# Kernel tuning notes

Measured on AMD Instinct MI355X. Metric: run time of the kernel, lower is better.

The kernel has to match this reference:

```python
import jax, jax.numpy as jnp
import numpy as np

EPS = 1e-5
INF = 1e9
H, D = 16, 24  # no_heads, c_hidden

def layer_norm(x, w, b):
    mu = jnp.mean(x, axis=-1, keepdims=True)
    var = jnp.mean(jnp.square(x - mu), axis=-1, keepdims=True)
    return (x - mu) * jax.lax.rsqrt(var + EPS) * w + b

def setup_inputs() -> dict:
    key = jax.random.key(0)
    ks = jax.random.split(key, 12)
    B, N, Cq, Cz = 1, 1024, 384, 128
    s = 0.02
    return {
        "a": jax.random.normal(ks[0], (B, N, Cq), jnp.float32),
        "z": jax.random.normal(ks[1], (B, N, N, Cz), jnp.float32),
        "mask": jnp.ones((B, N), jnp.float32),
        "ln_a_w": jnp.ones((Cq,), jnp.float32),
        "ln_a_b": jnp.zeros((Cq,), jnp.float32),
        "ln_z_w": jnp.ones((Cz,), jnp.float32),
        "ln_z_b": jnp.zeros((Cz,), jnp.float32),
        "w_z": jax.random.normal(ks[2], (Cz, H), jnp.float32) * s,
        "wq": jax.random.normal(ks[3], (Cq, H * D), jnp.float32) * s,
        "wk": jax.random.normal(ks[4], (Cq, H * D), jnp.float32) * s,
        "wv": jax.random.normal(ks[5], (Cq, H * D), jnp.float32) * s,
        "wg": jax.random.normal(ks[6], (Cq, H * D), jnp.float32) * s,
        "bg": jnp.ones((H * D,), jnp.float32),
        "wo": jax.random.normal(ks[7], (H * D, Cq), jnp.float32) * s,
        "bo": jnp.zeros((Cq,), jnp.float32),
    }

def reference(a, z, mask, ln_a_w, ln_a_b, ln_z_w, ln_z_b, w_z, wq, wk, wv, wg, bg, wo, bo):
    B, N, Cq = a.shape
    a_ln = layer_norm(a, ln_a_w, ln_a_b)                      # [B,N,Cq]
    # pair bias: LN -> Linear(no bias) -> permute to [B,H,N,N]
    zb = layer_norm(z, ln_z_w, ln_z_b) @ w_z                  # [B,N,N,H]
    pair_bias = jnp.transpose(zb, (0, 3, 1, 2))               # [B,H,N,N]
    mask_bias = (INF * (mask - 1.0))[:, None, None, :]        # [B,1,1,N]
    q = (a_ln @ wq).reshape(B, N, H, D) * (D ** -0.5)
    k = (a_ln @ wk).reshape(B, N, H, D)
    v = (a_ln @ wv).reshape(B, N, H, D)
    logits = jnp.einsum("bqhd,bkhd->bhqk", q, k) + mask_bias + pair_bias
    attn = jax.nn.softmax(logits, axis=-1)
    o = jnp.einsum("bhqk,bkhd->bqhd", attn, v)                # [B,N,H,D]
    g = jax.nn.sigmoid(a_ln @ wg + bg).reshape(B, N, H, D)
    o = (g * o).reshape(B, N, H * D)
    return o @ wo + bo
```

## Files before the change

### kernel.cpp

```cpp
#include <hip/hip_runtime.h>
#include <hip/hip_bf16.h>

typedef float f32x4 __attribute__((ext_vector_type(4)));
typedef short s16x8 __attribute__((ext_vector_type(8)));

__device__ __forceinline__ unsigned short f2bf(float x){
  unsigned u = __float_as_uint(x);
  u += 0x7fffu + ((u >> 16) & 1u);
  return (unsigned short)(u >> 16);
}
__device__ __forceinline__ float bf2f(unsigned short h){
  return __uint_as_float(((unsigned)h) << 16);
}
__device__ __forceinline__ unsigned pk_bf(float a, float b){
  __hip_bfloat162 t = __float22bfloat162_rn(make_float2(a, b));
  return *reinterpret_cast<unsigned*>(&t);
}

__global__ __launch_bounds__(256) void prep_kernel(const float* __restrict__ a, const float* __restrict__ ln_a_w,
                             const float* __restrict__ ln_a_b, const float* __restrict__ lnzw,
                             const float* __restrict__ lnzb, const float* __restrict__ w_z,
                             const float* __restrict__ wq, const float* __restrict__ wk,
                             const float* __restrict__ wv, const float* __restrict__ wg,
                             const float* __restrict__ wo,
                             unsigned short* __restrict__ a_lnB, unsigned short* __restrict__ wBall,
                             unsigned short* __restrict__ wwB, float* __restrict__ TU,
                             unsigned short* __restrict__ qTp, unsigned short* __restrict__ kTp,
                             unsigned short* __restrict__ vTt){
  int bid = blockIdx.x, tid = threadIdx.x;
  if (bid < 180){
    __shared__ float t[64][65];
    int mat = bid/36, tt = bid - mat*36;
    int c0 = (tt % 6)*64, k0 = (tt / 6)*64;
    const float* src = mat == 0 ? wq : mat == 1 ? wk : mat == 2 ? wv : mat == 3 ? wg : wo;
    int r = tid >> 4, c4 = (tid & 15)*4;
    #pragma unroll
    for (int rr = 0; rr < 4; ++rr){
      float4 v = *(const float4*)(src + (size_t)(k0 + r + rr*16)*384 + c0 + c4);
      t[r + rr*16][c4+0] = v.x; t[r + rr*16][c4+1] = v.y;
      t[r + rr*16][c4+2] = v.z; t[r + rr*16][c4+3] = v.w;
    }
    __syncthreads();
    float scale = (mat == 0) ? 0.20412414523193154f : 1.f;
    int cc = tid >> 2, kp = (tid & 3)*16;
    unsigned ow[8];
    #pragma unroll
    for (int j = 0; j < 8; ++j)
      ow[j] = pk_bf(t[kp + 2*j][cc]*scale, t[kp + 2*j + 1][cc]*scale);
    unsigned short* dst = wBall + ((size_t)(mat*384 + c0 + cc)*384 + k0 + kp);
    *(uint4*)dst       = make_uint4(ow[0], ow[1], ow[2], ow[3]);
    *(uint4*)(dst + 8) = make_uint4(ow[4], ow[5], ow[6], ow[7]);
  } else if (bid < 436){
    int r = (bid - 180)*4 + (tid >> 6), l = tid & 63;
    const float* ap = a + (size_t)r*384;
    float x[6]; float s = 0.f, sq = 0.f;
    #pragma unroll
    for (int i = 0; i < 6; ++i){ x[i] = ap[i*64 + l]; s += x[i]; sq += x[i]*x[i]; }
    #pragma unroll
    for (int off = 32; off; off >>= 1){ s += __shfl_xor(s, off); sq += __shfl_xor(sq, off); }
    float mu = s*(1.f/384.f);
    float var = sq*(1.f/384.f) - mu*mu;
    float rs = rsqrtf(var + 1e-5f);
    #pragma unroll
    for (int i = 0; i < 6; ++i){ int c = i*64 + l; a_lnB[(size_t)r*384 + c] = f2bf((x[i]-mu)*rs*ln_a_w[c] + ln_a_b[c]); }
  } else if (bid == 436){
    if (tid < 128){
      float lw = lnzw[tid];
      #pragma unroll
      for (int h = 0; h < 16; ++h) wwB[tid*16 + h] = f2bf(lw * w_z[tid*16 + h]);
    }
    if (tid < 16){
      float T = 0.f, U = 0.f;
      for (int c = 0; c < 128; ++c){ T += lnzw[c]*w_z[c*16 + tid]; U += lnzb[c]*w_z[c*16 + tid]; }
      TU[tid] = T; TU[16 + tid] = U;
    }
  } else {
    int t = (bid - 437)*256 + tid;
    uint4 zv = make_uint4(0,0,0,0);
    if (t < 16384)      *(uint4*)(qTp + (size_t)t*32 + 24) = zv;
    else if (t < 32768) *(uint4*)(kTp + (size_t)(t - 16384)*32 + 24) = zv;
    else {
      int t2 = t - 32768;
      int h = t2 >> 10, w = t2 & 1023;
      *(uint4*)(vTt + ((size_t)h*32 + 24)*1024 + (size_t)w*8) = zv;
    }
  }
}

__global__ __launch_bounds__(256) void midfuse_kernel(const unsigned short* __restrict__ AB,
                                                      const unsigned short* __restrict__ wBt,
                                                      const float* __restrict__ bg,
                                                      unsigned short* __restrict__ qTp, unsigned short* __restrict__ kTp,
                                                      unsigned short* __restrict__ vTt, float* __restrict__ g,
                                                      const float* __restrict__ z, const unsigned short* __restrict__ wwB,
                                                      const float* __restrict__ TU, const float* __restrict__ mask,
                                                      unsigned short* __restrict__ pbM){
  __shared__ char smem[16384];
  int bid = blockIdx.x, tid = threadIdx.x;
  int wave = tid >> 6, lane = tid & 63, l15 = lane & 15, sub = lane >> 4;
  if (bid < 384){
    s16x8* Al8 = (s16x8*)smem;
    s16x8* Bl8 = (s16x8*)(smem + 8192);
    int bx = bid % 24, by = bid / 24;
    int n0 = bx*64, m0 = by*64;
    f32x4 acc[4];
    #pragma unroll
    for (int c = 0; c < 4; ++c) acc[c] = (f32x4){0.f,0.f,0.f,0.f};
    const s16x8* Ag = (const s16x8*)AB;
    const s16x8* Bg = (const s16x8*)wBt;
    for (int ks = 0; ks < 6; ++ks){
      int k0u = ks*8;
      #pragma unroll
      for (int j = 0; j < 2; ++j){
        int idx = tid*2 + j;
        int row = idx >> 3, u = idx & 7;
        Al8[row*8 + (u ^ (row & 7))] = Ag[(size_t)(m0 + row)*48 + k0u + u];
        Bl8[row*8 + (u ^ (row & 7))] = Bg[(size_t)(n0 + row)*48 + k0u + u];
      }
      __syncthreads();
      #pragma unroll
      for (int kk = 0; kk < 2; ++kk){
        int arow = wave*16 + l15;
        s16x8 af = Al8[arow*8 + ((kk*4 + sub) ^ (arow & 7))];
        #pragma unroll
        for (int c = 0; c < 4; ++c){
          int brow = c*16 + l15;
          s16x8 bf = Bl8[brow*8 + ((kk*4 + sub) ^ (brow & 7))];
          acc[c] = __builtin_amdgcn_mfma_f32_16x16x32_bf16(af, bf, acc[c], 0, 0, 0);
        }
      }
      __syncthreads();
    }
    int which = bx / 6;
    int cb = n0 - which*384;
    if (which == 3){
      #pragma unroll
      for (int c = 0; c < 4; ++c){
        int col = cb + c*16 + l15;
        #pragma unroll
        for (int r = 0; r < 4; ++r){
          int row = m0 + wave*16 + sub*4 + r;
          float t = acc[c][r] + bg[col];
          g[(size_t)row*384 + col] = 1.f/(1.f + __expf(-t));
        }
      }
    } else if (which == 2){
      #pragma unroll
      for (int c = 0; c < 4; ++c){
        int col = cb + c*16 + l15;
        int h = col/24, d = col - h*24;
        unsigned p0 = pk_bf(acc[c][0], acc[c][1]);
        unsigned p1 = pk_bf(acc[c][2], acc[c][3]);
        size_t base = ((size_t)h*32 + d)*1024 + (size_t)(m0 + wave*16 + sub*4);
        *(uint2*)(vTt + base) = make_uint2(p0, p1);
      }
    } else {
      unsigned short* dst = which == 0 ? qTp : kTp;
      #pragma unroll
      for (int c = 0; c < 4; ++c){
        int col = cb + c*16 + l15;
        int h = col/24, d = col - h*24;
        #pragma unroll
        for (int r = 0; r < 4; ++r){
          int row = m0 + wave*16 + sub*4 + r;
          dst[((size_t)(h << 10) + row)*32 + d] = f2bf(acc[c][r]);
        }
      }
    }
  } else {
    float* sums = (float*)smem;
    float* sqs  = sums + 64;
    float (*accT)[17] = (float(*)[17])(sqs + 64);
    int tb = bid - 384;
    int h = l15, subz = sub;
    s16x8 bfr[4];
    #pragma unroll
    for (int kc = 0; kc < 4; ++kc)
      #pragma unroll
      for (int j = 0; j < 8; ++j) bfr[kc][j] = (short)wwB[(kc*32 + subz*8 + j)*16 + h];
    s16x8 ones1;
    #pragma unroll
    for (int j = 0; j < 8; ++j) ones1[j] = (h == 0) ? (short)0x3F80 : (short)0;
    int eh = tid >> 4, epl0 = (tid & 15)*4;
    float Te = TU[eh], Ue = TU[16 + eh];
    int row = wave*16 + h;
    for (int it = 0; it < 4; ++it){
      int tile = tb + it*4096;
      size_t pairBase = (size_t)tile*64;
      const float* zrow = z + (pairBase + row)*128;
      f32x4 acc  = {0.f, 0.f, 0.f, 0.f};
      f32x4 accS = {0.f, 0.f, 0.f, 0.f};
      f32x4 accG = {0.f, 0.f, 0.f, 0.f};
      #pragma unroll
      for (int kc = 0; kc < 4; ++kc){
        f32x4 v0 = *(const f32x4*)(zrow + kc*32 + subz*8);
        f32x4 v1 = *(const f32x4*)(zrow + kc*32 + subz*8 + 4);
        union { unsigned u[4]; s16x8 s; } cv;
        cv.u[0] = pk_bf(v0.x, v0.y); cv.u[1] = pk_bf(v0.z, v0.w);
        cv.u[2] = pk_bf(v1.x, v1.y); cv.u[3] = pk_bf(v1.z, v1.w);
        s16x8 af = cv.s;
        acc  = __builtin_amdgcn_mfma_f32_16x16x32_bf16(af, bfr[kc], acc, 0, 0, 0);
        accS = __builtin_amdgcn_mfma_f32_16x16x32_bf16(af, ones1, accS, 0, 0, 0);
        accG = __builtin_amdgcn_mfma_f32_16x16x32_bf16(af, af, accG, 0, 0, 0);
      }
      #pragma unroll
      for (int r = 0; r < 4; ++r) accT[wave*16 + subz*4 + r][h] = acc[r];
      if (h == 0){
        #pragma unroll
        for (int r = 0; r < 4; ++r) sums[wave*16 + subz*4 + r] = accS[r];
      }
      if (subz == (h >> 2)){
        int r = h & 3;
        float vq = r == 0 ? accG[0] : r == 1 ? accG[1] : r == 2 ? accG[2] : accG[3];
        sqs[wave*16 + h] = vq;
      }
      __syncthreads();
      float mus[4], rss[4];
      #pragma unroll
      for (int rr = 0; rr < 4; ++rr){
        float mu = sums[epl0+rr]*(1.f/128.f);
        float var = sqs[epl0+rr]*(1.f/128.f) - mu*mu;
        mus[rr] = mu; rss[rr] = rsqrtf(var + 1e-5f);
      }
      size_t p0 = pairBase + epl0;
      int q = (int)(p0 >> 10), k0 = (int)(p0 & 1023);
      float4 mk = *(const float4*)(mask + k0);
      float bv[4];
      bv[0] = rss[0]*(accT[epl0+0][eh] - mus[0]*Te) + Ue + 1e9f*(mk.x - 1.f);
      bv[1] = rss[1]*(accT[epl0+1][eh] - mus[1]*Te) + Ue + 1e9f*(mk.y - 1.f);
      bv[2] = rss[2]*(accT[epl0+2][eh] - mus[2]*Te) + Ue + 1e9f*(mk.z - 1.f);
      bv[3] = rss[3]*(accT[epl0+3][eh] - mus[3]*Te) + Ue + 1e9f*(mk.w - 1.f);
      int qb = q >> 6, q64 = q & 63;
      int qg = q64 >> 4, subq = (q64 >> 2) & 3, rr2 = q64 & 3;
      int kkt = k0 >> 6, c = (k0 >> 4) & 3, l15k = k0 & 15;
      size_t cbase = ((((size_t)(eh*16 + qb)*16 + kkt)*4 + qg)*4 + c)*256 + (size_t)rr2;
      #pragma unroll
      for (int i = 0; i < 4; ++i)
        pbM[cbase + (size_t)(subq*16 + l15k + i)*4] = f2bf(bv[i]);
      __syncthreads();
    }
  }
}

__global__ __launch_bounds__(512) void attn_kernel(const unsigned short* __restrict__ qTp, const unsigned short* __restrict__ kTp,
                                                   const unsigned short* __restrict__ vTt, const unsigned short* __restrict__ pbM,
                                                   const float* __restrict__ g, unsigned short* __restrict__ ogB){
  __shared__ float lds[8192];
  int tid = threadIdx.x;
  int wave = tid >> 6, lane = tid & 63, l15 = lane & 15, sub = lane >> 4;
  int qb32 = blockIdx.x, h = blockIdx.y;
  int qg_l = wave & 1, kkq = wave >> 1;
  int qrow = qb32*32 + qg_l*16 + l15;
  s16x8 qf = *(const s16x8*)(qTp + ((size_t)(h << 10) + qrow)*32 + sub*8);
  f32x4 o0 = {0.f,0.f,0.f,0.f}, o1 = {0.f,0.f,0.f,0.f};
  float m[4] = {-1e30f,-1e30f,-1e30f,-1e30f}, l[4] = {0.f,0.f,0.f,0.f};
  char* Pb = (char*)(lds + wave*1024);
  const unsigned short* kBase = kTp + ((size_t)(h << 10))*32;
  const unsigned short* vBase = vTt + (size_t)h*32*1024;
  int qb64 = qb32 >> 1, qg4 = (qb32 & 1)*2 + qg_l;
  const unsigned short* pbW = pbM + (size_t)(h*16 + qb64)*16*4096 + (size_t)qg4*1024 + (size_t)lane*4;
  for (int t = 0; t < 4; ++t){
    int kkt = kkq*4 + t;
    int kk0 = kkt*64;
    const unsigned short* pbt = pbW + (size_t)kkt*4096;
    uint2 pv0 = *(const uint2*)(pbt + 0);
    uint2 pv1 = *(const uint2*)(pbt + 256);
    uint2 pv2 = *(const uint2*)(pbt + 512);
    uint2 pv3 = *(const uint2*)(pbt + 768);
    f32x4 s[4];
    #pragma unroll
    for (int c = 0; c < 4; ++c){
      s16x8 kf = *(const s16x8*)(kBase + (size_t)(kk0 + c*16 + l15)*32 + sub*8);
      s[c] = __builtin_amdgcn_mfma_f32_16x16x32_bf16(qf, kf, (f32x4){0.f,0.f,0.f,0.f}, 0, 0, 0);
    }
    {
      uint2 pv[4] = {pv0, pv1, pv2, pv3};
      #pragma unroll
      for (int c = 0; c < 4; ++c){
        s[c][0] += bf2f((unsigned short)(pv[c].x & 0xffff));
        s[c][1] += bf2f((unsigned short)(pv[c].x >> 16));
        s[c][2] += bf2f((unsigned short)(pv[c].y & 0xffff));
        s[c][3] += bf2f((unsigned short)(pv[c].y >> 16));
      }
    }
    #pragma unroll
    for (int r = 0; r < 4; ++r){
      float pm = fmaxf(fmaxf(s[0][r], s[1][r]), fmaxf(s[2][r], s[3][r]));
      pm = fmaxf(pm, __shfl_xor(pm, 1));
      pm = fmaxf(pm, __shfl_xor(pm, 2));
      pm = fmaxf(pm, __shfl_xor(pm, 4));
      pm = fmaxf(pm, __shfl_xor(pm, 8));
      float mn = fmaxf(m[r], pm);
      float corr = __expf(m[r] - mn);
      m[r] = mn;
      float ps = 0.f;
      #pragma unroll
      for (int c = 0; c < 4; ++c){ s[c][r] = __expf(s[c][r] - mn); ps += s[c][r]; }
      ps += __shfl_xor(ps, 1); ps += __shfl_xor(ps, 2);
      ps += __shfl_xor(ps, 4); ps += __shfl_xor(ps, 8);
      l[r] = l[r]*corr + ps;
      o0[r] *= corr; o1[r] *= corr;
    }
    #pragma unroll
    for (int c = 0; c < 4; ++c){
      #pragma unroll
      for (int r = 0; r < 4; ++r){
        int qq = sub*4 + r;
        int byte = ((qq*128 + (c*16 + l15)*2)) ^ ((qq & 7) << 4);
        *(short*)(Pb + byte) = (short)f2bf(s[c][r]);
      }
    }
    #pragma unroll
    for (int kh = 0; kh < 2; ++kh){
      int byteA = (l15*128 + kh*64 + sub*16) ^ ((l15 & 7) << 4);
      s16x8 pa = *(const s16x8*)(Pb + byteA);
      s16x8 vb0 = *(const s16x8*)(vBase + (size_t)l15*1024 + kk0 + kh*32 + sub*8);
      s16x8 vb1 = *(const s16x8*)(vBase + (size_t)(16 + l15)*1024 + kk0 + kh*32 + sub*8);
      o0 = __builtin_amdgcn_mfma_f32_16x16x32_bf16(pa, vb0, o0, 0, 0, 0);
      o1 = __builtin_amdgcn_mfma_f32_16x16x32_bf16(pa, vb1, o1, 0, 0, 0);
    }
  }
  {
    float* cw = lds + wave*1024 + lane*16;
    cw[0] = o0[0]; cw[1] = o0[1]; cw[2] = o0[2]; cw[3] = o0[3];
    cw[4] = o1[0]; cw[5] = o1[1]; cw[6] = o1[2]; cw[7] = o1[3];
    cw[8] = m[0]; cw[9] = m[1]; cw[10] = m[2]; cw[11] = m[3];
    cw[12] = l[0]; cw[13] = l[1]; cw[14] = l[2]; cw[15] = l[3];
  }
  __syncthreads();
  if (kkq == 0){
    #pragma unroll
    for (int k2 = 1; k2 < 4; ++k2){
      const float* c2 = lds + (size_t)(k2*2 + qg_l)*1024 + lane*16;
      #pragma unroll
      for (int r = 0; r < 4; ++r){
        float m2 = c2[8 + r], l2 = c2[12 + r];
        float nm = fmaxf(m[r], m2);
        float f1 = __expf(m[r] - nm), f2 = __expf(m2 - nm);
        l[r] = l[r]*f1 + l2*f2;
        o0[r] = o0[r]*f1 + c2[r]*f2;
        o1[r] = o1[r]*f1 + c2[4 + r]*f2;
        m[r] = nm;
      }
    }
    #pragma unroll
    for (int r = 0; r < 4; ++r){
      float inv = 1.f/l[r];
      int q = qb32*32 + qg_l*16 + sub*4 + r;
      size_t base = (size_t)q*384 + h*24;
      ogB[base + l15] = f2bf(g[base + l15]*o0[r]*inv);
      if (l15 < 8) ogB[base + 16 + l15] = f2bf(g[base + 16 + l15]*o1[r]*inv);
    }
  }
}

__global__ __launch_bounds__(256) void gemm_out(const unsigned short* __restrict__ AB,
                                                const unsigned short* __restrict__ wBo,
                                                const float* __restrict__ bo, float* __restrict__ dst){
  __shared__ short Al[64*8*8];
  __shared__ short Bl[64*8*8];
  int tid = threadIdx.x;
  int wave = tid >> 6, lane = tid & 63, l15 = lane & 15, sub = lane >> 4;
  int n0 = blockIdx.x*64, m0 = blockIdx.y*64;
  f32x4 acc[4];
  #pragma unroll
  for (int c = 0; c < 4; ++c) acc[c] = (f32x4){0.f,0.f,0.f,0.f};
  const s16x8* Ag = (const s16x8*)AB;
  const s16x8* Bg = (const s16x8*)wBo;
  s16x8* Al8 = (s16x8*)Al; s16x8* Bl8 = (s16x8*)Bl;
  for (int ks = 0; ks < 6; ++ks){
    int k0u = ks*8;
    #pragma unroll
    for (int j = 0; j < 2; ++j){
      int idx = tid*2 + j;
      int row = idx >> 3, u = idx & 7;
      Al8[row*8 + (u ^ (row & 7))] = Ag[(size_t)(m0 + row)*48 + k0u + u];
      Bl8[row*8 + (u ^ (row & 7))] = Bg[(size_t)(n0 + row)*48 + k0u + u];
    }
    __syncthreads();
    #pragma unroll
    for (int kk = 0; kk < 2; ++kk){
      int arow = wave*16 + l15;
      s16x8 af = Al8[arow*8 + ((kk*4 + sub) ^ (arow & 7))];
      #pragma unroll
      for (int c = 0; c < 4; ++c){
        int brow = c*16 + l15;
        s16x8 bf = Bl8[brow*8 + ((kk*4 + sub) ^ (brow & 7))];
        acc[c] = __builtin_amdgcn_mfma_f32_16x16x32_bf16(af, bf, acc[c], 0, 0, 0);
      }
    }
    __syncthreads();
  }
  #pragma unroll
  for (int c = 0; c < 4; ++c){
    int col = n0 + c*16 + l15;
    float b = bo[col];
    #pragma unroll
    for (int r = 0; r < 4; ++r){
      int row = m0 + wave*16 + sub*4 + r;
      dst[(size_t)row*384 + col] = acc[c][r] + b;
    }
  }
}

extern "C" void kernel_launch(void* const* d_in, const int* in_sizes, int n_in,
                              void* d_out, int out_size, void* d_ws, size_t ws_size,
                              hipStream_t stream){
  const float* a      = (const float*)d_in[0];
  const float* z      = (const float*)d_in[1];
  const float* mask   = (const float*)d_in[2];
  const float* ln_a_w = (const float*)d_in[3];
  const float* ln_a_b = (const float*)d_in[4];
  const float* ln_z_w = (const float*)d_in[5];
  const float* ln_z_b = (const float*)d_in[6];
  const float* w_z    = (const float*)d_in[7];
  const float* wq     = (const float*)d_in[8];
  const float* wk     = (const float*)d_in[9];
  const float* wv     = (const float*)d_in[10];
  const float* wg     = (const float*)d_in[11];
  const float* bg     = (const float*)d_in[12];
  const float* wo     = (const float*)d_in[13];
  const float* bo     = (const float*)d_in[14];

  char* ws = (char*)d_ws;
  unsigned short* a_lnB = (unsigned short*)(ws + ((size_t)0u));
  unsigned short* wBall = (unsigned short*)(ws + ((size_t)1u << 20));
  unsigned short* qTp   = (unsigned short*)(ws + ((size_t)4u << 20));
  unsigned short* kTp   = (unsigned short*)(ws + ((size_t)6u << 20));
  unsigned short* vTt   = (unsigned short*)(ws + ((size_t)8u << 20));
  float* g    = (float*)(ws + ((size_t)10u << 20));
  unsigned short* ogB = (unsigned short*)(ws + ((size_t)12u << 20));
  unsigned short* wwB = (unsigned short*)(ws + ((size_t)14u << 20));
  float* TU   = (float*)(ws + ((size_t)14u << 20) + 8192);
  unsigned short* pbM = (unsigned short*)(ws + ((size_t)24u << 20));

  hipLaunchKernelGGL(prep_kernel, dim3(629), dim3(256), 0, stream, a, ln_a_w, ln_a_b,
                     ln_z_w, ln_z_b, w_z, wq, wk, wv, wg, wo, a_lnB, wBall, wwB, TU, qTp, kTp, vTt);
  hipLaunchKernelGGL(midfuse_kernel, dim3(4480), dim3(256), 0, stream, a_lnB, wBall, bg,
                     qTp, kTp, vTt, g, z, wwB, TU, mask, pbM);
  hipLaunchKernelGGL(attn_kernel, dim3(32,16), dim3(512), 0, stream, qTp, kTp, vTt, pbM, g, ogB);
  hipLaunchKernelGGL(gemm_out, dim3(6,16), dim3(256), 0, stream, ogB, wBall + (size_t)4*384*384, bo, (float*)d_out);
}
```

Baseline: 173.6 us.

## Split fused projection/pair-bias kernel and retile z bias for packed stores

Splits the combined midfuse kernel into a separate QKVG projection GEMM and a pair-bias kernel. The new z-bias kernel tiles 4 query rows by 16 keys, so each thread writes four bias values for its head as one packed 8-byte store instead of four scattered 2-byte stores. The attention kernel now loads the K fragments for the next key tile one iteration ahead and fully unrolls the loop. The cost is one extra kernel launch, the loss of overlap between the small GEMM and the large z pass, and more registers held in the attention kernel.

```diff
diff --git a/kernel.cpp b/kernel.cpp
--- a/kernel.cpp
+++ b/kernel.cpp
@@ -87,158 +87,150 @@
   }
 }
 
-__global__ __launch_bounds__(256) void midfuse_kernel(const unsigned short* __restrict__ AB,
-                                                      const unsigned short* __restrict__ wBt,
-                                                      const float* __restrict__ bg,
-                                                      unsigned short* __restrict__ qTp, unsigned short* __restrict__ kTp,
-                                                      unsigned short* __restrict__ vTt, float* __restrict__ g,
-                                                      const float* __restrict__ z, const unsigned short* __restrict__ wwB,
-                                                      const float* __restrict__ TU, const float* __restrict__ mask,
-                                                      unsigned short* __restrict__ pbM){
-  __shared__ char smem[16384];
-  int bid = blockIdx.x, tid = threadIdx.x;
+__global__ __launch_bounds__(256) void qkvg_kernel(const unsigned short* __restrict__ AB,
+                                                   const unsigned short* __restrict__ wBt,
+                                                   const float* __restrict__ bg,
+                                                   unsigned short* __restrict__ qTp, unsigned short* __restrict__ kTp,
+                                                   unsigned short* __restrict__ vTt, float* __restrict__ g){
+  __shared__ short Al[64*8*8];
+  __shared__ short Bl[64*8*8];
+  int tid = threadIdx.x;
   int wave = tid >> 6, lane = tid & 63, l15 = lane & 15, sub = lane >> 4;
-  if (bid < 384){
-    s16x8* Al8 = (s16x8*)smem;
-    s16x8* Bl8 = (s16x8*)(smem + 8192);
-    int bx = bid % 24, by = bid / 24;
-    int n0 = bx*64, m0 = by*64;
-    f32x4 acc[4];
-    #pragma unroll
-    for (int c = 0; c < 4; ++c) acc[c] = (f32x4){0.f,0.f,0.f,0.f};
-    const s16x8* Ag = (const s16x8*)AB;
-    const s16x8* Bg = (const s16x8*)wBt;
-    for (int ks = 0; ks < 6; ++ks){
-      int k0u = ks*8;
-      #pragma unroll
-      for (int j = 0; j < 2; ++j){
-        int idx = tid*2 + j;
-        int row = idx >> 3, u = idx & 7;
-        Al8[row*8 + (u ^ (row & 7))] = Ag[(size_t)(m0 + row)*48 + k0u + u];
-        Bl8[row*8 + (u ^ (row & 7))] = Bg[(size_t)(n0 + row)*48 + k0u + u];
-      }
-      __syncthreads();
-      #pragma unroll
-      for (int kk = 0; kk < 2; ++kk){
-        int arow = wave*16 + l15;
-        s16x8 af = Al8[arow*8 + ((kk*4 + sub) ^ (arow & 7))];
-        #pragma unroll
-        for (int c = 0; c < 4; ++c){
-          int brow = c*16 + l15;
-          s16x8 bf = Bl8[brow*8 + ((kk*4 + sub) ^ (brow & 7))];
-          acc[c] = __builtin_amdgcn_mfma_f32_16x16x32_bf16(af, bf, acc[c], 0, 0, 0);
-        }
-      }
-      __syncthreads();
-    }
-    int which = bx / 6;
-    int cb = n0 - which*384;
-    if (which == 3){
+  int n0 = blockIdx.x*64, m0 = blockIdx.y*64;
+  f32x4 acc[4];
+  #pragma unroll
+  for (int c = 0; c < 4; ++c) acc[c] = (f32x4){0.f,0.f,0.f,0.f};
+  const s16x8* Ag = (const s16x8*)AB;
+  const s16x8* Bg = (const s16x8*)wBt;
+  s16x8* Al8 = (s16x8*)Al; s16x8* Bl8 = (s16x8*)Bl;
+  for (int ks = 0; ks < 6; ++ks){
+    int k0u = ks*8;
+    #pragma unroll
+    for (int j = 0; j < 2; ++j){
+      int idx = tid*2 + j;
+      int row = idx >> 3, u = idx & 7;
+      Al8[row*8 + (u ^ (row & 7))] = Ag[(size_t)(m0 + row)*48 + k0u + u];
+      Bl8[row*8 + (u ^ (row & 7))] = Bg[(size_t)(n0 + row)*48 + k0u + u];
+    }
+    __syncthreads();
+    #pragma unroll
+    for (int kk = 0; kk < 2; ++kk){
+      int arow = wave*16 + l15;
+      s16x8 af = Al8[arow*8 + ((kk*4 + sub) ^ (arow & 7))];
       #pragma unroll
       for (int c = 0; c < 4; ++c){
-        int col = cb + c*16 + l15;
-        #pragma unroll
-        for (int r = 0; r < 4; ++r){
-          int row = m0 + wave*16 + sub*4 + r;
-          float t = acc[c][r] + bg[col];
-          g[(size_t)row*384 + col] = 1.f/(1.f + __expf(-t));
-        }
-      }
-    } else if (which == 2){
-      #pragma unroll
-      for (int c = 0; c < 4; ++c){
-        int col = cb + c*16 + l15;
-        int h = col/24, d = col - h*24;
-        unsigned p0 = pk_bf(acc[c][0], acc[c][1]);
-        unsigned p1 = pk_bf(acc[c][2], acc[c][3]);
-        size_t base = ((size_t)h*32 + d)*1024 + (size_t)(m0 + wave*16 + sub*4);
-        *(uint2*)(vTt + base) = make_uint2(p0, p1);
-      }
-    } else {
-      unsigned short* dst = which == 0 ? qTp : kTp;
-      #pragma unroll
-      for (int c = 0; c < 4; ++c){
-        int col = cb + c*16 + l15;
-        int h = col/24, d = col - h*24;
-        #pragma unroll
-        for (int r = 0; r < 4; ++r){
-          int row = m0 + wave*16 + sub*4 + r;
-          dst[((size_t)(h << 10) + row)*32 + d] = f2bf(acc[c][r]);
-        }
-      }
+        int brow = c*16 + l15;
+        s16x8 bf = Bl8[brow*8 + ((kk*4 + sub) ^ (brow & 7))];
+        acc[c] = __builtin_amdgcn_mfma_f32_16x16x32_bf16(af, bf, acc[c], 0, 0, 0);
+      }
+    }
+    __syncthreads();
+  }
+  int which = blockIdx.x / 6;
+  int cb = n0 - which*384;
+  if (which == 3){
+    #pragma unroll
+    for (int c = 0; c < 4; ++c){
+      int col = cb + c*16 + l15;
+      #pragma unroll
+      for (int r = 0; r < 4; ++r){
+        int row = m0 + wave*16 + sub*4 + r;
+        float t = acc[c][r] + bg[col];
+        g[(size_t)row*384 + col] = 1.f/(1.f + __expf(-t));
+      }
+    }
+  } else if (which == 2){
+    #pragma unroll
+    for (int c = 0; c < 4; ++c){
+      int col = cb + c*16 + l15;
+      int h = col/24, d = col - h*24;
+      unsigned p0 = pk_bf(acc[c][0], acc[c][1]);
+      unsigned p1 = pk_bf(acc[c][2], acc[c][3]);
+      size_t base = ((size_t)h*32 + d)*1024 + (size_t)(m0 + wave*16 + sub*4);
+      *(uint2*)(vTt + base) = make_uint2(p0, p1);
     }
   } else {
-    float* sums = (float*)smem;
-    float* sqs  = sums + 64;
-    float (*accT)[17] = (float(*)[17])(sqs + 64);
-    int tb = bid - 384;
-    int h = l15, subz = sub;
-    s16x8 bfr[4];
-    #pragma unroll
-    for (int kc = 0; kc < 4; ++kc)
-      #pragma unroll
-      for (int j = 0; j < 8; ++j) bfr[kc][j] = (short)wwB[(kc*32 + subz*8 + j)*16 + h];
-    s16x8 ones1;
-    #pragma unroll
-    for (int j = 0; j < 8; ++j) ones1[j] = (h == 0) ? (short)0x3F80 : (short)0;
-    int eh = tid >> 4, epl0 = (tid & 15)*4;
-    float Te = TU[eh], Ue = TU[16 + eh];
-    int row = wave*16 + h;
-    for (int it = 0; it < 4; ++it){
-      int tile = tb + it*4096;
-      size_t pairBase = (size_t)tile*64;
-      const float* zrow = z + (pairBase + row)*128;
-      f32x4 acc  = {0.f, 0.f, 0.f, 0.f};
-      f32x4 accS = {0.f, 0.f, 0.f, 0.f};
-      f32x4 accG = {0.f, 0.f, 0.f, 0.f};
-      #pragma unroll
-      for (int kc = 0; kc < 4; ++kc){
-        f32x4 v0 = *(const f32x4*)(zrow + kc*32 + subz*8);
-        f32x4 v1 = *(const f32x4*)(zrow + kc*32 + subz*8 + 4);
-        union { unsigned u[4]; s16x8 s; } cv;
-        cv.u[0] = pk_bf(v0.x, v0.y); cv.u[1] = pk_bf(v0.z, v0.w);
-        cv.u[2] = pk_bf(v1.x, v1.y); cv.u[3] = pk_bf(v1.z, v1.w);
-        s16x8 af = cv.s;
-        acc  = __builtin_amdgcn_mfma_f32_16x16x32_bf16(af, bfr[kc], acc, 0, 0, 0);
-        accS = __builtin_amdgcn_mfma_f32_16x16x32_bf16(af, ones1, accS, 0, 0, 0);
-        accG = __builtin_amdgcn_mfma_f32_16x16x32_bf16(af, af, accG, 0, 0, 0);
-      }
-      #pragma unroll
-      for (int r = 0; r < 4; ++r) accT[wave*16 + subz*4 + r][h] = acc[r];
-      if (h == 0){
-        #pragma unroll
-        for (int r = 0; r < 4; ++r) sums[wave*16 + subz*4 + r] = accS[r];
-      }
-      if (subz == (h >> 2)){
-        int r = h & 3;
-        float vq = r == 0 ? accG[0] : r == 1 ? accG[1] : r == 2 ? accG[2] : accG[3];
-        sqs[wave*16 + h] = vq;
-      }
-      __syncthreads();
-      float mus[4], rss[4];
-      #pragma unroll
-      for (int rr = 0; rr < 4; ++rr){
-        float mu = sums[epl0+rr]*(1.f/128.f);
-        float var = sqs[epl0+rr]*(1.f/128.f) - mu*mu;
-        mus[rr] = mu; rss[rr] = rsqrtf(var + 1e-5f);
-      }
-      size_t p0 = pairBase + epl0;
-      int q = (int)(p0 >> 10), k0 = (int)(p0 & 1023);
-      float4 mk = *(const float4*)(mask + k0);
-      float bv[4];
-      bv[0] = rss[0]*(accT[epl0+0][eh] - mus[0]*Te) + Ue + 1e9f*(mk.x - 1.f);
-      bv[1] = rss[1]*(accT[epl0+1][eh] - mus[1]*Te) + Ue + 1e9f*(mk.y - 1.f);
-      bv[2] = rss[2]*(accT[epl0+2][eh] - mus[2]*Te) + Ue + 1e9f*(mk.z - 1.f);
-      bv[3] = rss[3]*(accT[epl0+3][eh] - mus[3]*Te) + Ue + 1e9f*(mk.w - 1.f);
-      int qb = q >> 6, q64 = q & 63;
-      int qg = q64 >> 4, subq = (q64 >> 2) & 3, rr2 = q64 & 3;
-      int kkt = k0 >> 6, c = (k0 >> 4) & 3, l15k = k0 & 15;
-      size_t cbase = ((((size_t)(eh*16 + qb)*16 + kkt)*4 + qg)*4 + c)*256 + (size_t)rr2;
-      #pragma unroll
-      for (int i = 0; i < 4; ++i)
-        pbM[cbase + (size_t)(subq*16 + l15k + i)*4] = f2bf(bv[i]);
-      __syncthreads();
-    }
+    unsigned short* dst = which == 0 ? qTp : kTp;
+    #pragma unroll
+    for (int c = 0; c < 4; ++c){
+      int col = cb + c*16 + l15;
+      int h = col/24, d = col - h*24;
+      #pragma unroll
+      for (int r = 0; r < 4; ++r){
+        int row = m0 + wave*16 + sub*4 + r;
+        dst[((size_t)(h << 10) + row)*32 + d] = f2bf(acc[c][r]);
+      }
+    }
+  }
+}
+
+__global__ __launch_bounds__(256) void zbias_kernel(const float* __restrict__ z, const unsigned short* __restrict__ wwB,
+                                                    const float* __restrict__ TU, const float* __restrict__ mask,
+                                                    unsigned short* __restrict__ pbM){
+  __shared__ float sums[64];
+  __shared__ float sqs[64];
+  __shared__ float accT[64][17];
+  int tid = threadIdx.x;
+  int wave = tid >> 6, lane = tid & 63;
+  int h = lane & 15, sub = lane >> 4;
+  s16x8 bfr[4];
+  #pragma unroll
+  for (int kc = 0; kc < 4; ++kc)
+    #pragma unroll
+    for (int j = 0; j < 8; ++j) bfr[kc][j] = (short)wwB[(kc*32 + sub*8 + j)*16 + h];
+  s16x8 ones1;
+  #pragma unroll
+  for (int j = 0; j < 8; ++j) ones1[j] = (h == 0) ? (short)0x3F80 : (short)0;
+  int eh = tid >> 4, ej = tid & 15;
+  float Te = TU[eh], Ue = TU[16 + eh];
+  for (int it = 0; it < 4; ++it){
+    int tile = blockIdx.x + it*4096;
+    int qt = tile >> 6, kt = tile & 63;
+    int q0 = qt*4, k0 = kt*16;
+    const float* zrow = z + ((size_t)(q0 + wave)*1024 + k0 + h)*128;
+    f32x4 acc  = {0.f, 0.f, 0.f, 0.f};
+    f32x4 accS = {0.f, 0.f, 0.f, 0.f};
+    f32x4 accG = {0.f, 0.f, 0.f, 0.f};
+    #pragma unroll
+    for (int kc = 0; kc < 4; ++kc){
+      f32x4 v0 = *(const f32x4*)(zrow + kc*32 + sub*8);
+      f32x4 v1 = *(const f32x4*)(zrow + kc*32 + sub*8 + 4);
+      union { unsigned u[4]; s16x8 s; } cv;
+      cv.u[0] = pk_bf(v0.x, v0.y); cv.u[1] = pk_bf(v0.z, v0.w);
+      cv.u[2] = pk_bf(v1.x, v1.y); cv.u[3] = pk_bf(v1.z, v1.w);
+      s16x8 af = cv.s;
+      acc  = __builtin_amdgcn_mfma_f32_16x16x32_bf16(af, bfr[kc], acc, 0, 0, 0);
+      accS = __builtin_amdgcn_mfma_f32_16x16x32_bf16(af, ones1, accS, 0, 0, 0);
+      accG = __builtin_amdgcn_mfma_f32_16x16x32_bf16(af, af, accG, 0, 0, 0);
+    }
+    #pragma unroll
+    for (int r = 0; r < 4; ++r) accT[wave*16 + sub*4 + r][h] = acc[r];
+    if (h == 0){
+      #pragma unroll
+      for (int r = 0; r < 4; ++r) sums[wave*16 + sub*4 + r] = accS[r];
+    }
+    if (sub == (h >> 2)){
+      int r = h & 3;
+      float vq = r == 0 ? accG[0] : r == 1 ? accG[1] : r == 2 ? accG[2] : accG[3];
+      sqs[wave*16 + h] = vq;
+    }
+    __syncthreads();
+    int k = k0 + ej;
+    float mb = 1e9f*(mask[k] - 1.f);
+    unsigned short pv[4];
+    #pragma unroll
+    for (int i = 0; i < 4; ++i){
+      int row = i*16 + ej;
+      float mu = sums[row]*(1.f/128.f);
+      float var = sqs[row]*(1.f/128.f) - mu*mu;
+      float rs = rsqrtf(var + 1e-5f);
+      pv[i] = f2bf(rs*(accT[row][eh] - mu*Te) + Ue + mb);
+    }
+    int qb = q0 >> 6, qg = (q0 >> 4) & 3, subq = (q0 >> 2) & 3;
+    int kkt = k >> 6, c = (k >> 4) & 3, l15k = k & 15;
+    size_t off = ((((size_t)(eh*16 + qb)*16 + kkt)*4 + qg)*4 + c)*256 + (size_t)(subq*16 + l15k)*4;
+    *(uint2*)(pbM + off) = make_uint2(((unsigned)pv[1] << 16) | pv[0], ((unsigned)pv[3] << 16) | pv[2]);
+    __syncthreads();
   }
 }
 
@@ -259,6 +251,15 @@
   const unsigned short* vBase = vTt + (size_t)h*32*1024;
   int qb64 = qb32 >> 1, qg4 = (qb32 & 1)*2 + qg_l;
   const unsigned short* pbW = pbM + (size_t)(h*16 + qb64)*16*4096 + (size_t)qg4*1024 + (size_t)lane*4;
+  s16x8 kfA0, kfA1, kfA2, kfA3;
+  {
+    int kk0 = (kkq*4)*64;
+    kfA0 = *(const s16x8*)(kBase + (size_t)(kk0 +  0 + l15)*32 + sub*8);
+    kfA1 = *(const s16x8*)(kBase + (size_t)(kk0 + 16 + l15)*32 + sub*8);
+    kfA2 = *(const s16x8*)(kBase + (size_t)(kk0 + 32 + l15)*32 + sub*8);
+    kfA3 = *(const s16x8*)(kBase + (size_t)(kk0 + 48 + l15)*32 + sub*8);
+  }
+  #pragma unroll
   for (int t = 0; t < 4; ++t){
     int kkt = kkq*4 + t;
     int kk0 = kkt*64;
@@ -268,10 +269,16 @@
     uint2 pv2 = *(const uint2*)(pbt + 512);
     uint2 pv3 = *(const uint2*)(pbt + 768);
     f32x4 s[4];
-    #pragma unroll
-    for (int c = 0; c < 4; ++c){
-      s16x8 kf = *(const s16x8*)(kBase + (size_t)(kk0 + c*16 + l15)*32 + sub*8);
-      s[c] = __builtin_amdgcn_mfma_f32_16x16x32_bf16(qf, kf, (f32x4){0.f,0.f,0.f,0.f}, 0, 0, 0);
+    s[0] = __builtin_amdgcn_mfma_f32_16x16x32_bf16(qf, kfA0, (f32x4){0.f,0.f,0.f,0.f}, 0, 0, 0);
+    s[1] = __builtin_amdgcn_mfma_f32_16x16x32_bf16(qf, kfA1, (f32x4){0.f,0.f,0.f,0.f}, 0, 0, 0);
+    s[2] = __builtin_amdgcn_mfma_f32_16x16x32_bf16(qf, kfA2, (f32x4){0.f,0.f,0.f,0.f}, 0, 0, 0);
+    s[3] = __builtin_amdgcn_mfma_f32_16x16x32_bf16(qf, kfA3, (f32x4){0.f,0.f,0.f,0.f}, 0, 0, 0);
+    if (t < 3){
+      int nk = kk0 + 64;
+      kfA0 = *(const s16x8*)(kBase + (size_t)(nk +  0 + l15)*32 + sub*8);
+      kfA1 = *(const s16x8*)(kBase + (size_t)(nk + 16 + l15)*32 + sub*8);
+      kfA2 = *(const s16x8*)(kBase + (size_t)(nk + 32 + l15)*32 + sub*8);
+      kfA3 = *(const s16x8*)(kBase + (size_t)(nk + 48 + l15)*32 + sub*8);
     }
     {
       uint2 pv[4] = {pv0, pv1, pv2, pv3};
@@ -436,8 +443,8 @@
 
   hipLaunchKernelGGL(prep_kernel, dim3(629), dim3(256), 0, stream, a, ln_a_w, ln_a_b,
                      ln_z_w, ln_z_b, w_z, wq, wk, wv, wg, wo, a_lnB, wBall, wwB, TU, qTp, kTp, vTt);
-  hipLaunchKernelGGL(midfuse_kernel, dim3(4480), dim3(256), 0, stream, a_lnB, wBall, bg,
-                     qTp, kTp, vTt, g, z, wwB, TU, mask, pbM);
+  hipLaunchKernelGGL(qkvg_kernel, dim3(24,16), dim3(256), 0, stream, a_lnB, wBall, bg, qTp, kTp, vTt, g);
+  hipLaunchKernelGGL(zbias_kernel, dim3(4096), dim3(256), 0, stream, z, wwB, TU, mask, pbM);
   hipLaunchKernelGGL(attn_kernel, dim3(32,16), dim3(512), 0, stream, qTp, kTp, vTt, pbM, g, ogB);
   hipLaunchKernelGGL(gemm_out, dim3(6,16), dim3(256), 0, stream, ogB, wBall + (size_t)4*384*384, bo, (float*)d_out);
 }
```

Result: faster. 161.5 us (-7.0%).
